# Optimization experiments

Hardware: AMD Instinct MI355X
Metric: run time of the kernel (lower is better)

Reference implementation:

```python
import jax, jax.numpy as jnp
import numpy as np

EMB = 1024
HEADS = 16
HEAD_DIM = EMB // HEADS


def setup_inputs() -> dict:
    key = jax.random.key(0)
    ks = jax.random.split(key, 7)
    B, Sq, Sk = 4, 1024, 1024
    dp_emb = jax.random.normal(ks[0], (B, Sq, EMB), dtype=jnp.float32)
    dp_mask = jnp.ones((B, 1, 1, Sq), dtype=jnp.float32)
    K = jax.random.normal(ks[1], (B, HEADS, Sk, HEAD_DIM), dtype=jnp.float32)
    V = jax.random.normal(ks[2], (B, HEADS, Sk, HEAD_DIM), dtype=jnp.float32)
    M = jax.random.normal(ks[3], (B, HEADS, Sq, Sk), dtype=jnp.float32)
    # query Linear params (key/value Linears in the torch module are unused)
    Wq = jax.random.normal(ks[4], (EMB, EMB), dtype=jnp.float32) / np.sqrt(EMB)
    bq = jax.random.normal(ks[5], (EMB,), dtype=jnp.float32) * 0.01
    return {"dp_emb": dp_emb, "dp_mask": dp_mask, "K": K, "V": V, "M": M, "Wq": Wq, "bq": bq}


def reference(dp_emb, dp_mask, K, V, M, Wq, bq):
    B, Sq, E = dp_emb.shape
    H, d = HEADS, HEAD_DIM
    # query projection: nn.Linear -> x @ W.T + b
    q = dp_emb @ Wq.T + bq                                  # [B,Sq,E]
    q = q.reshape(B, Sq, H, d).transpose(0, 2, 1, 3)        # [B,H,Sq,d]
    scores = jnp.einsum('bhqd,bhkd->bhqk', q, K) / np.sqrt(d).astype(jnp.float32)
    scores = scores - M                                      # additive mask (subtraction)
    probs = jax.nn.softmax(scores, axis=-1)                  # [B,H,Sq,Sk]
    # (probs.T * dp_mask).T == probs * dp_mask reshaped to mask the query axis
    probs = probs * jnp.swapaxes(dp_mask, -1, -2)            # dp_mask [B,1,1,Sq] -> [B,1,Sq,1]
    target_score = jnp.sum(jnp.max(probs, axis=2), axis=1)   # [B,Sk]
    # dropout omitted (eval/inference semantics)
    ctx = jnp.einsum('bhqk,bhkd->bhqd', probs, V)            # [B,H,Sq,d]
    ctx = ctx.transpose(0, 2, 1, 3).reshape(B, Sq, E)
    return ctx, target_score
```

## Files before the change

### kernel.cpp

```cpp
#include <hip/hip_runtime.h>

#define B_ 4
#define H_ 16
#define SQ 1024
#define SK 1024
#define DHD 64
#define E_ 1024

typedef _Float16 half_t;
typedef __attribute__((ext_vector_type(8))) _Float16 half8;
typedef __attribute__((ext_vector_type(4))) float f32x4;

static __device__ __forceinline__ f32x4 mfma16h(half8 a, half8 b, f32x4 c) {
  return __builtin_amdgcn_mfma_f32_16x16x32_f16(a, b, c, 0, 0, 0);
}

__global__ __launch_bounds__(256) void cvt_kernel(const float* __restrict__ src,
                                                  half_t* __restrict__ dst, int n8) {
  int i = blockIdx.x * 256 + threadIdx.x;
  if (i >= n8) return;
  f32x4 v0 = *(const f32x4*)(src + (size_t)i * 8);
  f32x4 v1 = *(const f32x4*)(src + (size_t)i * 8 + 4);
  half8 h;
#pragma unroll
  for (int j = 0; j < 4; ++j) {
    h[j] = (half_t)v0[j];
    h[4 + j] = (half_t)v1[j];
  }
  *(half8*)(dst + (size_t)i * 8) = h;
}

__global__ __launch_bounds__(256) void vtrans_kernel(const float* __restrict__ V,
                                                     half_t* __restrict__ vt) {
  __shared__ float tile[64][65];
  int bh = blockIdx.x >> 4;
  int kt = blockIdx.x & 15;
  int tid = threadIdx.x;
  const float* src = V + ((size_t)bh * SK + (size_t)kt * 64) * DHD;
#pragma unroll
  for (int i = 0; i < 16; ++i) {
    int idx = i * 256 + tid;
    tile[idx >> 6][idx & 63] = src[idx];
  }
  __syncthreads();
#pragma unroll
  for (int i = 0; i < 16; ++i) {
    int idx = i * 256 + tid;
    int d = idx >> 6, kk = idx & 63;
    vt[((size_t)bh * DHD + d) * SK + kt * 64 + kk] = (half_t)tile[kk][d];
  }
}

__global__ __launch_bounds__(256) void proj_kernel(const half_t* __restrict__ emb,
                                                   const half_t* __restrict__ wq,
                                                   const float* __restrict__ bq,
                                                   half_t* __restrict__ qh) {
  int tid = threadIdx.x, wid = tid >> 6, lane = tid & 63;
  int lr = lane & 15, lg = lane >> 4;
  int m0 = blockIdx.y * 64 + (wid >> 1) * 32;
  int n0 = blockIdx.x * 64 + (wid & 1) * 32;
  f32x4 acc[2][2];
#pragma unroll
  for (int i = 0; i < 2; ++i)
#pragma unroll
    for (int j = 0; j < 2; ++j) acc[i][j] = (f32x4){0.f, 0.f, 0.f, 0.f};

  for (int kk = 0; kk < E_; kk += 32) {
    half8 a[2], b[2];
#pragma unroll
    for (int g = 0; g < 2; ++g) {
      a[g] = *(const half8*)(emb + (size_t)(m0 + g * 16 + lr) * E_ + kk + lg * 8);
      b[g] = *(const half8*)(wq + (size_t)(n0 + g * 16 + lr) * E_ + kk + lg * 8);
    }
#pragma unroll
    for (int i = 0; i < 2; ++i)
#pragma unroll
      for (int j = 0; j < 2; ++j) acc[i][j] = mfma16h(a[i], b[j], acc[i][j]);
  }
#pragma unroll
  for (int i = 0; i < 2; ++i)
#pragma unroll
    for (int j = 0; j < 2; ++j)
#pragma unroll
      for (int r = 0; r < 4; ++r) {
        int m = m0 + i * 16 + lg * 4 + r;
        int n = n0 + j * 16 + lr;
        float v = (acc[i][j][r] + bq[n]) * 0.125f;
        int b = m >> 10, sq = m & 1023, h = n >> 6, dd = n & 63;
        qh[((size_t)(b * H_ + h) * SQ + sq) * DHD + dd] = (half_t)v;
      }
}

__global__ __launch_bounds__(512, 4) void attn_kernel(const half_t* __restrict__ qh,
                                                      const half_t* __restrict__ kh,
                                                      const half_t* __restrict__ vt,
                                                      const float* __restrict__ M,
                                                      const float* __restrict__ dpm,
                                                      float* __restrict__ out,
                                                      int* __restrict__ colmax) {
  __shared__ half_t panel[32][1032];
  __shared__ float wred[8][32];
  __shared__ float gmaxs[32];
  __shared__ float rowscale[32];

  int bid = blockIdx.x;
  int x = bid & 7, j = bid >> 3;
  int bh = (x << 3) | (j >> 5);
  int q0 = (j & 31) << 5;
  int b = bh >> 4, h = bh & 15;

  int tid = threadIdx.x, wid = tid >> 6, lane = tid & 63;
  int lr = lane & 15, lg = lane >> 4;
  int c0 = wid * 128;

  half8 aq[2][2];
#pragma unroll
  for (int qg = 0; qg < 2; ++qg)
#pragma unroll
    for (int dh = 0; dh < 2; ++dh)
      aq[qg][dh] = *(const half8*)(qh + ((size_t)bh * SQ + q0 + qg * 16 + lr) * DHD +
                                   dh * 32 + lg * 8);

  const float* mp[2][4];
#pragma unroll
  for (int qg = 0; qg < 2; ++qg)
#pragma unroll
    for (int r = 0; r < 4; ++r)
      mp[qg][r] = M + ((size_t)bh * SQ + q0 + qg * 16 + lg * 4 + r) * SK + c0 + lr;

  f32x4 S[2][8];
#pragma unroll
  for (int kt = 0; kt < 8; ++kt) {
    int col = c0 + kt * 16 + lr;
    const half_t* kr = kh + ((size_t)bh * SK + col) * DHD;
    half8 b0 = *(const half8*)(kr + lg * 8);
    half8 b1 = *(const half8*)(kr + 32 + lg * 8);
#pragma unroll
    for (int qg = 0; qg < 2; ++qg) {
      f32x4 acc = (f32x4){0.f, 0.f, 0.f, 0.f};
      acc = mfma16h(aq[qg][0], b0, acc);
      acc = mfma16h(aq[qg][1], b1, acc);
      f32x4 mv;
#pragma unroll
      for (int r = 0; r < 4; ++r) mv[r] = mp[qg][r][kt * 16];
      S[qg][kt] = acc - mv;
    }
  }

  float mx[2][4];
#pragma unroll
  for (int qg = 0; qg < 2; ++qg)
#pragma unroll
    for (int r = 0; r < 4; ++r) {
      float m0 = S[qg][0][r];
#pragma unroll
      for (int kt = 1; kt < 8; ++kt) m0 = fmaxf(m0, S[qg][kt][r]);
#pragma unroll
      for (int off = 1; off < 16; off <<= 1) m0 = fmaxf(m0, __shfl_xor(m0, off));
      mx[qg][r] = m0;
    }
  if (lr == 0) {
#pragma unroll
    for (int qg = 0; qg < 2; ++qg)
#pragma unroll
      for (int r = 0; r < 4; ++r) wred[wid][qg * 16 + lg * 4 + r] = mx[qg][r];
  }
  __syncthreads();
  if (tid < 32) {
    float g = wred[0][tid];
#pragma unroll
    for (int w = 1; w < 8; ++w) g = fmaxf(g, wred[w][tid]);
    gmaxs[tid] = g;
  }
  __syncthreads();

  float g[2][4];
#pragma unroll
  for (int qg = 0; qg < 2; ++qg)
#pragma unroll
    for (int r = 0; r < 4; ++r) g[qg][r] = gmaxs[qg * 16 + lg * 4 + r];
  float sm[2][4] = {{0.f, 0.f, 0.f, 0.f}, {0.f, 0.f, 0.f, 0.f}};
#pragma unroll
  for (int qg = 0; qg < 2; ++qg)
#pragma unroll
    for (int kt = 0; kt < 8; ++kt)
#pragma unroll
      for (int r = 0; r < 4; ++r) {
        float p = __expf(S[qg][kt][r] - g[qg][r]);
        panel[qg * 16 + lg * 4 + r][c0 + kt * 16 + lr] = (half_t)p;
        sm[qg][r] += p;
      }
#pragma unroll
  for (int qg = 0; qg < 2; ++qg)
#pragma unroll
    for (int r = 0; r < 4; ++r) {
#pragma unroll
      for (int off = 1; off < 16; off <<= 1) sm[qg][r] += __shfl_xor(sm[qg][r], off);
    }
  if (lr == 0) {
#pragma unroll
    for (int qg = 0; qg < 2; ++qg)
#pragma unroll
      for (int r = 0; r < 4; ++r) wred[wid][qg * 16 + lg * 4 + r] = sm[qg][r];
  }
  __syncthreads();
  if (tid < 32) {
    float ls = 0.f;
#pragma unroll
    for (int w = 0; w < 8; ++w) ls += wred[w][tid];
    rowscale[tid] = dpm[b * SQ + q0 + tid] / ls;
  }
  __syncthreads();

  for (int c = tid; c < SK; c += 512) {
    float cm = 0.f;
#pragma unroll 8
    for (int r = 0; r < 32; ++r) cm = fmaxf(cm, (float)panel[r][c] * rowscale[r]);
    atomicMax(colmax + (size_t)bh * SK + c, __float_as_int(cm));
  }

  int qgw = wid >> 2, dg = wid & 3;
  const half_t* vrow = vt + ((size_t)bh * DHD + dg * 16 + lr) * SK;
  f32x4 acc = (f32x4){0.f, 0.f, 0.f, 0.f};
  for (int ks = 0; ks < SK; ks += 32) {
    half8 pa = *(const half8*)&panel[qgw * 16 + lr][ks + lg * 8];
    half8 vb = *(const half8*)(vrow + ks + lg * 8);
    acc = mfma16h(pa, vb, acc);
  }
#pragma unroll
  for (int r = 0; r < 4; ++r) {
    int rt = qgw * 16 + lg * 4 + r;
    out[((size_t)b * SQ + q0 + rt) * E_ + h * DHD + dg * 16 + lr] = acc[r] * rowscale[rt];
  }
}

__global__ __launch_bounds__(256) void tscore_kernel(const int* __restrict__ colmax,
                                                     float* __restrict__ out) {
  int g = blockIdx.x * 256 + threadIdx.x;
  int b = g >> 10, k = g & 1023;
  float s = 0.f;
#pragma unroll
  for (int hh = 0; hh < H_; ++hh) s += __int_as_float(colmax[((b * H_ + hh) << 10) + k]);
  out[(size_t)B_ * SQ * E_ + g] = s;
}

extern "C" void kernel_launch(void* const* d_in, const int* in_sizes, int n_in,
                              void* d_out, int out_size, void* d_ws, size_t ws_size,
                              hipStream_t stream) {
  const float* dp_emb = (const float*)d_in[0];
  const float* dp_mask = (const float*)d_in[1];
  const float* K = (const float*)d_in[2];
  const float* V = (const float*)d_in[3];
  const float* M = (const float*)d_in[4];
  const float* Wq = (const float*)d_in[5];
  const float* bq = (const float*)d_in[6];
  float* out = (float*)d_out;

  char* ws = (char*)d_ws;
  half_t* q_h = (half_t*)(ws);
  half_t* k_h = (half_t*)(ws + (8ull << 20));
  half_t* vt_h = (half_t*)(ws + (16ull << 20));
  half_t* emb_h = (half_t*)(ws + (24ull << 20));
  half_t* wq_h = (half_t*)(ws + (33ull << 20));
  int* colmax = (int*)(ws + (36ull << 20));

  hipMemsetAsync(colmax, 0, (size_t)B_ * H_ * SK * sizeof(int), stream);
  cvt_kernel<<<(B_ * SQ * E_ / 8 + 255) / 256, 256, 0, stream>>>(dp_emb, emb_h, B_ * SQ * E_ / 8);
  cvt_kernel<<<(E_ * E_ / 8 + 255) / 256, 256, 0, stream>>>(Wq, wq_h, E_ * E_ / 8);
  cvt_kernel<<<(B_ * H_ * SK * DHD / 8 + 255) / 256, 256, 0, stream>>>(K, k_h,
                                                                       B_ * H_ * SK * DHD / 8);
  vtrans_kernel<<<B_ * H_ * 16, 256, 0, stream>>>(V, vt_h);
  proj_kernel<<<dim3(E_ / 64, (B_ * SQ) / 64), 256, 0, stream>>>(emb_h, wq_h, bq, q_h);
  attn_kernel<<<B_ * H_ * (SQ / 32), 512, 0, stream>>>(q_h, k_h, vt_h, M, dp_mask, out, colmax);
  tscore_kernel<<<(B_ * SK) / 256, 256, 0, stream>>>(colmax, out);
}
```

Before: 239.2 us.

## Restructure attention tiles: 16-row blocks, transposed MFMA, negated K, swizzled panel

The attention kernel now processes 16 query rows per 256-thread block instead of 32 rows per 512 threads. It computes the transposed score tile (K times Q) so the mask M can be loaded as contiguous float4 directly into the MFMA accumulator. K is pre-negated during conversion so the accumulator holds M minus scores, and the softmax uses a row minimum with exp(g - T). The probability panel uses an XOR-swizzled shared layout to cut bank conflicts, and column-max and output stores are vectorised. The aim is to make the M loads coalesced and remove the separate subtract, at the cost of twice as many blocks and reloading K and V per 16 rows.

```diff
diff --git a/kernel.cpp b/kernel.cpp
--- a/kernel.cpp
+++ b/kernel.cpp
@@ -9,12 +9,14 @@
 
 typedef _Float16 half_t;
 typedef __attribute__((ext_vector_type(8))) _Float16 half8;
+typedef __attribute__((ext_vector_type(4))) _Float16 half4;
 typedef __attribute__((ext_vector_type(4))) float f32x4;
 
 static __device__ __forceinline__ f32x4 mfma16h(half8 a, half8 b, f32x4 c) {
   return __builtin_amdgcn_mfma_f32_16x16x32_f16(a, b, c, 0, 0, 0);
 }
 
+template <int NEG>
 __global__ __launch_bounds__(256) void cvt_kernel(const float* __restrict__ src,
                                                   half_t* __restrict__ dst, int n8) {
   int i = blockIdx.x * 256 + threadIdx.x;
@@ -24,8 +26,8 @@
   half8 h;
 #pragma unroll
   for (int j = 0; j < 4; ++j) {
-    h[j] = (half_t)v0[j];
-    h[4 + j] = (half_t)v1[j];
+    h[j] = (half_t)(NEG ? -v0[j] : v0[j]);
+    h[4 + j] = (half_t)(NEG ? -v1[j] : v1[j]);
   }
   *(half8*)(dst + (size_t)i * 8) = h;
 }
@@ -91,147 +93,111 @@
       }
 }
 
-__global__ __launch_bounds__(512, 4) void attn_kernel(const half_t* __restrict__ qh,
-                                                      const half_t* __restrict__ kh,
+__global__ __launch_bounds__(256, 4) void attn_kernel(const half_t* __restrict__ qh,
+                                                      const half_t* __restrict__ khn,
                                                       const half_t* __restrict__ vt,
                                                       const float* __restrict__ M,
                                                       const float* __restrict__ dpm,
                                                       float* __restrict__ out,
                                                       int* __restrict__ colmax) {
-  __shared__ half_t panel[32][1032];
-  __shared__ float wred[8][32];
-  __shared__ float gmaxs[32];
-  __shared__ float rowscale[32];
+  __shared__ char panel[16 * 2048];
+  __shared__ float wred[4][16];
+  __shared__ float gred[16];
+  __shared__ float rowscale[16];
 
   int bid = blockIdx.x;
   int x = bid & 7, j = bid >> 3;
-  int bh = (x << 3) | (j >> 5);
-  int q0 = (j & 31) << 5;
+  int bh = x * 8 + (j >> 6);
+  int q0 = (j & 63) << 4;
   int b = bh >> 4, h = bh & 15;
 
   int tid = threadIdx.x, wid = tid >> 6, lane = tid & 63;
   int lr = lane & 15, lg = lane >> 4;
-  int c0 = wid * 128;
-
-  half8 aq[2][2];
-#pragma unroll
-  for (int qg = 0; qg < 2; ++qg)
-#pragma unroll
-    for (int dh = 0; dh < 2; ++dh)
-      aq[qg][dh] = *(const half8*)(qh + ((size_t)bh * SQ + q0 + qg * 16 + lr) * DHD +
-                                   dh * 32 + lg * 8);
-
-  const float* mp[2][4];
-#pragma unroll
-  for (int qg = 0; qg < 2; ++qg)
-#pragma unroll
-    for (int r = 0; r < 4; ++r)
-      mp[qg][r] = M + ((size_t)bh * SQ + q0 + qg * 16 + lg * 4 + r) * SK + c0 + lr;
-
-  f32x4 S[2][8];
-#pragma unroll
-  for (int kt = 0; kt < 8; ++kt) {
-    int col = c0 + kt * 16 + lr;
-    const half_t* kr = kh + ((size_t)bh * SK + col) * DHD;
-    half8 b0 = *(const half8*)(kr + lg * 8);
-    half8 b1 = *(const half8*)(kr + 32 + lg * 8);
-#pragma unroll
-    for (int qg = 0; qg < 2; ++qg) {
-      f32x4 acc = (f32x4){0.f, 0.f, 0.f, 0.f};
-      acc = mfma16h(aq[qg][0], b0, acc);
-      acc = mfma16h(aq[qg][1], b1, acc);
-      f32x4 mv;
-#pragma unroll
-      for (int r = 0; r < 4; ++r) mv[r] = mp[qg][r][kt * 16];
-      S[qg][kt] = acc - mv;
+  int kc0 = wid * 256;
+
+  const float* mrow = M + ((size_t)bh * SQ + q0 + lr) * SK + kc0 + lg * 4;
+  f32x4 T[16];
+#pragma unroll
+  for (int kt = 0; kt < 16; ++kt) T[kt] = *(const f32x4*)(mrow + kt * 16);
+
+  const half_t* qrow = qh + ((size_t)bh * SQ + q0 + lr) * DHD;
+  half8 qf0 = *(const half8*)(qrow + lg * 8);
+  half8 qf1 = *(const half8*)(qrow + 32 + lg * 8);
+
+#pragma unroll
+  for (int kt = 0; kt < 16; ++kt) {
+    const half_t* krow = khn + ((size_t)bh * SK + kc0 + kt * 16 + lr) * DHD;
+    half8 k0 = *(const half8*)(krow + lg * 8);
+    half8 k1 = *(const half8*)(krow + 32 + lg * 8);
+    T[kt] = mfma16h(k0, qf0, T[kt]);
+    T[kt] = mfma16h(k1, qf1, T[kt]);
+  }
+
+  float mn = T[0][0];
+#pragma unroll
+  for (int kt = 0; kt < 16; ++kt)
+#pragma unroll
+    for (int r = 0; r < 4; ++r) mn = fminf(mn, T[kt][r]);
+  mn = fminf(mn, __shfl_xor(mn, 16));
+  mn = fminf(mn, __shfl_xor(mn, 32));
+  if (lg == 0) wred[wid][lr] = mn;
+  __syncthreads();
+  if (tid < 16)
+    gred[tid] = fminf(fminf(wred[0][tid], wred[1][tid]), fminf(wred[2][tid], wred[3][tid]));
+  __syncthreads();
+  float g = gred[lr];
+
+  float ssum = 0.f;
+#pragma unroll
+  for (int kt = 0; kt < 16; ++kt) {
+    half4 ph;
+#pragma unroll
+    for (int r = 0; r < 4; ++r) {
+      float p = __expf(g - T[kt][r]);
+      ssum += p;
+      ph[r] = (half_t)p;
     }
-  }
-
-  float mx[2][4];
-#pragma unroll
-  for (int qg = 0; qg < 2; ++qg)
-#pragma unroll
-    for (int r = 0; r < 4; ++r) {
-      float m0 = S[qg][0][r];
-#pragma unroll
-      for (int kt = 1; kt < 8; ++kt) m0 = fmaxf(m0, S[qg][kt][r]);
-#pragma unroll
-      for (int off = 1; off < 16; off <<= 1) m0 = fmaxf(m0, __shfl_xor(m0, off));
-      mx[qg][r] = m0;
+    int k = kc0 + kt * 16 + lg * 4;
+    *(half4*)(panel + ((lr * 2048 + k * 2) ^ ((lr & 7) << 4))) = ph;
+  }
+  ssum += __shfl_xor(ssum, 16);
+  ssum += __shfl_xor(ssum, 32);
+  if (lg == 0) wred[wid][lr] = ssum;
+  __syncthreads();
+  if (tid < 16)
+    rowscale[tid] =
+        dpm[b * SQ + q0 + tid] / (wred[0][tid] + wred[1][tid] + wred[2][tid] + wred[3][tid]);
+  __syncthreads();
+
+  {
+    int c0 = tid * 4;
+    f32x4 cm = (f32x4){0.f, 0.f, 0.f, 0.f};
+#pragma unroll
+    for (int r = 0; r < 16; ++r) {
+      half4 ph = *(const half4*)(panel + ((r * 2048 + c0 * 2) ^ ((r & 7) << 4)));
+      float rs = rowscale[r];
+#pragma unroll
+      for (int i = 0; i < 4; ++i) cm[i] = fmaxf(cm[i], (float)ph[i] * rs);
     }
-  if (lr == 0) {
-#pragma unroll
-    for (int qg = 0; qg < 2; ++qg)
-#pragma unroll
-      for (int r = 0; r < 4; ++r) wred[wid][qg * 16 + lg * 4 + r] = mx[qg][r];
-  }
-  __syncthreads();
-  if (tid < 32) {
-    float g = wred[0][tid];
-#pragma unroll
-    for (int w = 1; w < 8; ++w) g = fmaxf(g, wred[w][tid]);
-    gmaxs[tid] = g;
-  }
-  __syncthreads();
-
-  float g[2][4];
-#pragma unroll
-  for (int qg = 0; qg < 2; ++qg)
-#pragma unroll
-    for (int r = 0; r < 4; ++r) g[qg][r] = gmaxs[qg * 16 + lg * 4 + r];
-  float sm[2][4] = {{0.f, 0.f, 0.f, 0.f}, {0.f, 0.f, 0.f, 0.f}};
-#pragma unroll
-  for (int qg = 0; qg < 2; ++qg)
-#pragma unroll
-    for (int kt = 0; kt < 8; ++kt)
-#pragma unroll
-      for (int r = 0; r < 4; ++r) {
-        float p = __expf(S[qg][kt][r] - g[qg][r]);
-        panel[qg * 16 + lg * 4 + r][c0 + kt * 16 + lr] = (half_t)p;
-        sm[qg][r] += p;
-      }
-#pragma unroll
-  for (int qg = 0; qg < 2; ++qg)
-#pragma unroll
-    for (int r = 0; r < 4; ++r) {
-#pragma unroll
-      for (int off = 1; off < 16; off <<= 1) sm[qg][r] += __shfl_xor(sm[qg][r], off);
-    }
-  if (lr == 0) {
-#pragma unroll
-    for (int qg = 0; qg < 2; ++qg)
-#pragma unroll
-      for (int r = 0; r < 4; ++r) wred[wid][qg * 16 + lg * 4 + r] = sm[qg][r];
-  }
-  __syncthreads();
-  if (tid < 32) {
-    float ls = 0.f;
-#pragma unroll
-    for (int w = 0; w < 8; ++w) ls += wred[w][tid];
-    rowscale[tid] = dpm[b * SQ + q0 + tid] / ls;
-  }
-  __syncthreads();
-
-  for (int c = tid; c < SK; c += 512) {
-    float cm = 0.f;
+#pragma unroll
+    for (int i = 0; i < 4; ++i)
+      atomicMax(colmax + (size_t)bh * SK + c0 + i, __float_as_int(cm[i]));
+  }
+
+  int d0 = wid * 16;
+  const half_t* vrow = vt + ((size_t)bh * DHD + d0 + lr) * SK;
+  f32x4 acc = (f32x4){0.f, 0.f, 0.f, 0.f};
 #pragma unroll 8
-    for (int r = 0; r < 32; ++r) cm = fmaxf(cm, (float)panel[r][c] * rowscale[r]);
-    atomicMax(colmax + (size_t)bh * SK + c, __float_as_int(cm));
-  }
-
-  int qgw = wid >> 2, dg = wid & 3;
-  const half_t* vrow = vt + ((size_t)bh * DHD + dg * 16 + lr) * SK;
-  f32x4 acc = (f32x4){0.f, 0.f, 0.f, 0.f};
   for (int ks = 0; ks < SK; ks += 32) {
-    half8 pa = *(const half8*)&panel[qgw * 16 + lr][ks + lg * 8];
-    half8 vb = *(const half8*)(vrow + ks + lg * 8);
-    acc = mfma16h(pa, vb, acc);
-  }
-#pragma unroll
-  for (int r = 0; r < 4; ++r) {
-    int rt = qgw * 16 + lg * 4 + r;
-    out[((size_t)b * SQ + q0 + rt) * E_ + h * DHD + dg * 16 + lr] = acc[r] * rowscale[rt];
-  }
+    half8 av = *(const half8*)(vrow + ks + lg * 8);
+    half8 bp = *(const half8*)(panel + ((lr * 2048 + (ks + lg * 8) * 2) ^ ((lr & 7) << 4)));
+    acc = mfma16h(av, bp, acc);
+  }
+  float rs = rowscale[lr];
+  f32x4 res;
+#pragma unroll
+  for (int r = 0; r < 4; ++r) res[r] = acc[r] * rs;
+  *(f32x4*)(out + ((size_t)b * SQ + q0 + lr) * E_ + h * DHD + d0 + lg * 4) = res;
 }
 
 __global__ __launch_bounds__(256) void tscore_kernel(const int* __restrict__ colmax,
@@ -258,19 +224,21 @@
 
   char* ws = (char*)d_ws;
   half_t* q_h = (half_t*)(ws);
-  half_t* k_h = (half_t*)(ws + (8ull << 20));
+  half_t* k_hn = (half_t*)(ws + (8ull << 20));
   half_t* vt_h = (half_t*)(ws + (16ull << 20));
   half_t* emb_h = (half_t*)(ws + (24ull << 20));
-  half_t* wq_h = (half_t*)(ws + (33ull << 20));
-  int* colmax = (int*)(ws + (36ull << 20));
+  half_t* wq_h = (half_t*)(ws + (32ull << 20));
+  int* colmax = (int*)(ws + (35ull << 20));
 
   hipMemsetAsync(colmax, 0, (size_t)B_ * H_ * SK * sizeof(int), stream);
-  cvt_kernel<<<(B_ * SQ * E_ / 8 + 255) / 256, 256, 0, stream>>>(dp_emb, emb_h, B_ * SQ * E_ / 8);
-  cvt_kernel<<<(E_ * E_ / 8 + 255) / 256, 256, 0, stream>>>(Wq, wq_h, E_ * E_ / 8);
-  cvt_kernel<<<(B_ * H_ * SK * DHD / 8 + 255) / 256, 256, 0, stream>>>(K, k_h,
-                                                                       B_ * H_ * SK * DHD / 8);
+  cvt_kernel<0><<<(B_ * SQ * E_ / 8 + 255) / 256, 256, 0, stream>>>(dp_emb, emb_h,
+                                                                    B_ * SQ * E_ / 8);
+  cvt_kernel<0><<<(E_ * E_ / 8 + 255) / 256, 256, 0, stream>>>(Wq, wq_h, E_ * E_ / 8);
+  cvt_kernel<1><<<(B_ * H_ * SK * DHD / 8 + 255) / 256, 256, 0, stream>>>(
+      K, k_hn, B_ * H_ * SK * DHD / 8);
   vtrans_kernel<<<B_ * H_ * 16, 256, 0, stream>>>(V, vt_h);
   proj_kernel<<<dim3(E_ / 64, (B_ * SQ) / 64), 256, 0, stream>>>(emb_h, wq_h, bq, q_h);
-  attn_kernel<<<B_ * H_ * (SQ / 32), 512, 0, stream>>>(q_h, k_h, vt_h, M, dp_mask, out, colmax);
+  attn_kernel<<<B_ * H_ * (SQ / 16), 256, 0, stream>>>(q_h, k_hn, vt_h, M, dp_mask, out,
+                                                       colmax);
   tscore_kernel<<<(B_ * SK) / 256, 256, 0, stream>>>(colmax, out);
 }
```

Result: slower. 354.6 us (+48.2%).
